# Kernel optimization log

Measured on AMD Instinct MI355X. Metric: run time of the kernel, lower is better.

Reference implementation:

```python
import jax, jax.numpy as jnp
import numpy as np

INPUT_DIM, HID_DIM, OUTPUT_DIM, N = 256, 128, 256, 16384
SCALE = 128 ** (-0.5)


def setup_inputs() -> dict:
    key = jax.random.key(0)
    ks = jax.random.split(key, 11)
    s_in = 1.0 / np.sqrt(INPUT_DIM)
    s_hid = 1.0 / np.sqrt(HID_DIM)
    return {
        "q": jax.random.normal(ks[0], (N, INPUT_DIM), jnp.float32),
        "k": jax.random.normal(ks[1], (N, INPUT_DIM), jnp.float32),
        "v": jax.random.normal(ks[2], (N, INPUT_DIM), jnp.float32),
        "Wq": jax.random.uniform(ks[3], (INPUT_DIM, HID_DIM), jnp.float32, -s_in, s_in),
        "bq": jax.random.uniform(ks[4], (HID_DIM,), jnp.float32, -s_in, s_in),
        "Wk": jax.random.uniform(ks[5], (INPUT_DIM, HID_DIM), jnp.float32, -s_in, s_in),
        "bk": jax.random.uniform(ks[6], (HID_DIM,), jnp.float32, -s_in, s_in),
        "Wv": jax.random.uniform(ks[7], (INPUT_DIM, HID_DIM), jnp.float32, -s_in, s_in),
        "bv": jax.random.uniform(ks[8], (HID_DIM,), jnp.float32, -s_in, s_in),
        "Wo": jax.random.uniform(ks[9], (HID_DIM, OUTPUT_DIM), jnp.float32, -s_hid, s_hid),
        "bo": jax.random.uniform(ks[10], (OUTPUT_DIM,), jnp.float32, -s_hid, s_hid),
    }


def reference(q, k, v, Wq, bq, Wk, bk, Wv, bv, Wo, bo):
    qh = q @ Wq + bq                      # [N, H]
    kh = k @ Wk + bk                      # [N, H]
    vh = v @ Wv + bv                      # [N, H]
    scores = (qh @ kh.T) * SCALE          # [N, N] materialized as in original
    attn = jax.nn.softmax(scores, axis=-1)
    out = attn @ vh                       # [N, H]
    return out @ Wo + bo                  # [N, OUTPUT_DIM]
```

## Files before the change

### kernel.cpp

```cpp
#include <hip/hip_runtime.h>
#include <hip/hip_bf16.h>
#include <stdint.h>


#define N_TOK 16384
#define IN_DIM 256
#define HID 128
#define OUT_DIM 256
#define KVB 32
#define BM 128
#define TOT_TILES (N_TOK / KVB)

typedef __bf16   bf16x8 __attribute__((ext_vector_type(8)));
typedef short    short8 __attribute__((ext_vector_type(8)));
typedef float    f32x4  __attribute__((ext_vector_type(4)));
typedef float    f32x16 __attribute__((ext_vector_type(16)));
typedef uint32_t u32x2  __attribute__((ext_vector_type(2)));
typedef long     longx2 __attribute__((ext_vector_type(2)));

#define MFMA16(a,b,c) __builtin_amdgcn_mfma_f32_16x16x32_bf16((a),(b),(c),0,0,0)
#define MFMA8(a,b,c)  __builtin_amdgcn_mfma_f32_32x32x16_fp8_fp8((a),(b),(c),0,0,0)
#define EXP2(x) __builtin_amdgcn_exp2f(x)

__device__ __forceinline__ short f2bf(float f) {
    union { float f; uint32_t u; } v; v.f = f;
    uint32_t r = v.u + 0x7FFFu + ((v.u >> 16) & 1u);
    return (short)(r >> 16);
}

template <bool HI>
__device__ __forceinline__ uint32_t pk_fp8(float a, float b, uint32_t old) {
    return (uint32_t)__builtin_amdgcn_cvt_pk_fp8_f32(a, b, (int)old, HI);
}

__device__ __forceinline__ unsigned char f2fp8(float f) {
    return (unsigned char)(pk_fp8<false>(f, f, 0u) & 0xFFu);
}

__device__ __forceinline__ void pswap(uint32_t& a, uint32_t& b) {
    auto r = __builtin_amdgcn_permlane32_swap(a, b, false, false);
    a = r[0]; b = r[1];
}

__device__ __forceinline__ void gl16(const void* g, const void* l) {
    __builtin_amdgcn_global_load_lds(
        (const __attribute__((address_space(1))) void*)g,
        (__attribute__((address_space(3))) void*)l, 16, 0, 0);
}

__global__ void wt4_kernel(const float* __restrict__ Wq, const float* __restrict__ Wk,
                           const float* __restrict__ Wv, const float* __restrict__ Wo,
                           short* __restrict__ tq, short* __restrict__ tk,
                           short* __restrict__ tv, short* __restrict__ to_)
{
    int idx = blockIdx.x * 256 + threadIdx.x;
    int w = idx >> 15, i = idx & 32767;
    if (w < 3) {
        const float* W = (w == 0) ? Wq : (w == 1) ? Wk : Wv;
        short* T = (w == 0) ? tq : (w == 1) ? tk : tv;
        int k = i >> 7, c = i & 127;
        T[c * 256 + k] = f2bf(W[i]);
    } else {
        int k = i >> 8, c = i & 255;
        to_[c * 128 + k] = f2bf(Wo[i]);
    }
}

__global__ __launch_bounds__(256) void proj3_kernel(
    const float* __restrict__ q, const float* __restrict__ k, const float* __restrict__ v,
    const short* __restrict__ tq, const short* __restrict__ tk, const short* __restrict__ tv,
    const float* __restrict__ bq, const float* __restrict__ bk, const float* __restrict__ bv,
    unsigned char* __restrict__ qh, unsigned char* __restrict__ kh,
    unsigned char* __restrict__ vh)
{
    const int y = blockIdx.y;
    const float* X  = (y == 0) ? q  : (y == 1) ? k  : v;
    const short* WT = (y == 0) ? tq : (y == 1) ? tk : tv;
    const float* bias = (y == 0) ? bq : (y == 1) ? bk : bv;
    unsigned char* Y = (y == 0) ? qh : (y == 1) ? kh : vh;

    const int lane = threadIdx.x & 63;
    const int wave = threadIdx.x >> 6;
    const int g = lane >> 4, c = lane & 15;
    const int rowbase = blockIdx.x * 64 + wave * 16;

    bf16x8 a[8];
    const float* xrow = X + (size_t)(rowbase + c) * IN_DIM;
#pragma unroll
    for (int kk = 0; kk < 8; ++kk) {
        const float* p = xrow + kk * 32 + 8 * g;
        float4 f0 = *(const float4*)(p);
        float4 f1 = *(const float4*)(p + 4);
        short8 t;
        t[0]=f2bf(f0.x); t[1]=f2bf(f0.y); t[2]=f2bf(f0.z); t[3]=f2bf(f0.w);
        t[4]=f2bf(f1.x); t[5]=f2bf(f1.y); t[6]=f2bf(f1.z); t[7]=f2bf(f1.w);
        a[kk] = __builtin_bit_cast(bf16x8, t);
    }

    f32x4 acc[8];
#pragma unroll
    for (int nf = 0; nf < 8; ++nf) acc[nf] = (f32x4){0.f, 0.f, 0.f, 0.f};

#pragma unroll
    for (int kk = 0; kk < 8; ++kk) {
#pragma unroll
        for (int nf = 0; nf < 8; ++nf) {
            bf16x8 b = *(const bf16x8*)(WT + (size_t)(c + 16 * nf) * IN_DIM + kk * 32 + 8 * g);
            acc[nf] = MFMA16(a[kk], b, acc[nf]);
        }
    }

#pragma unroll
    for (int nf = 0; nf < 8; ++nf) {
        int col = c + 16 * nf;
        float bval = bias[col];
#pragma unroll
        for (int r = 0; r < 4; ++r) {
            int row = rowbase + 4 * g + r;
            unsigned char val = f2fp8(acc[nf][r] + bval);
            if (y == 0) {
                Y[(size_t)row * HID + col] = val;
            } else if (y == 1) {
                Y[(size_t)(row >> 5) * 4096 + (col >> 5) * 1024 + ((col >> 3) & 1) * 512
                  + (row & 31) * 16 + ((col >> 4) & 1) * 8 + (col & 7)] = val;
            } else {
                Y[(size_t)(row >> 5) * 4096 + (col >> 5) * 1024 + ((row >> 3) & 1) * 512
                  + (col & 31) * 16 + ((row >> 4) & 1) * 8 + (row & 7)] = val;
            }
        }
    }
}

__global__ __launch_bounds__(256, 3) void flash_kernel(
    const unsigned char* __restrict__ qh, const unsigned char* __restrict__ kh,
    const unsigned char* __restrict__ vh,
    short* __restrict__ Opart, float* __restrict__ Lpart,
    int nsplit)
{
    __shared__ __align__(16) unsigned char K_lds[3][KVB * HID];
    __shared__ __align__(16) unsigned char V_lds[3][KVB * HID];

    const float kSc = 0.088388347648318447f * 1.4426950408889634f;

    const int tid  = threadIdx.x;
    const int lane = tid & 63;
    const int wave = tid >> 6;
    const int hi   = lane >> 5;
    const int col  = lane & 31;

    const int lid = blockIdx.x;
    const int split = lid >> 7;
    const int qtile = lid & 127;

    const int qb = qtile * BM + wave * 32;
    const int tbase = TOT_TILES / nsplit, trem = TOT_TILES % nsplit;
    const int ntiles = tbase + (split < trem ? 1 : 0);
    const int ktile0 = tbase * split + (split < trem ? split : trem);

    long qf[8];
    const unsigned char* qrow = qh + (size_t)(qb + col) * HID + 8 * hi;
#pragma unroll
    for (int kk = 0; kk < 8; ++kk)
        qf[kk] = *(const long*)(qrow + 16 * kk);

    f32x16 o[4];
#pragma unroll
    for (int nf = 0; nf < 4; ++nf)
#pragma unroll
        for (int i = 0; i < 16; ++i) o[nf][i] = 0.f;
    float l_run = 0.f;

    const unsigned char* kbase = kh + (size_t)ktile0 * 4096;
    const unsigned char* vbase = vh + (size_t)ktile0 * 4096;
    const int lds_off = tid * 16;
    const int frag_off = hi * 512 + col * 16;

    auto stage = [&](int t, int buf) {
        gl16(kbase + (size_t)t * 4096 + lds_off, &K_lds[buf][lds_off]);
        gl16(vbase + (size_t)t * 4096 + lds_off, &V_lds[buf][lds_off]);
    };

    stage(0, 0);
    if (1 < ntiles) stage(1, 1); else stage(0, 1);
    asm volatile("s_waitcnt vmcnt(2)" ::: "memory");
    __builtin_amdgcn_s_barrier();

    for (int t = 0; t < ntiles; ++t) {
        const int cur = t % 3;
        if (t + 2 < ntiles) stage(t + 2, (t + 2) % 3);
        const unsigned char* Kc = &K_lds[cur][0];
        const unsigned char* Vc = &V_lds[cur][0];

        f32x16 s0;
#pragma unroll
        for (int i = 0; i < 16; ++i) s0[i] = 0.f;
        __builtin_amdgcn_s_setprio(1);
#pragma unroll
        for (int p = 0; p < 4; ++p) {
            longx2 kp = *(const longx2*)(Kc + p * 1024 + frag_off);
            s0 = MFMA8(kp[0], qf[2 * p],     s0);
            s0 = MFMA8(kp[1], qf[2 * p + 1], s0);
        }
        __builtin_amdgcn_s_setprio(0);

        long pa0, pa1;
        {
            float e[16];
#pragma unroll
            for (int i = 0; i < 16; ++i) e[i] = EXP2(s0[i] * kSc);
            l_run += (((e[0]+e[1])+(e[2]+e[3])) + ((e[4]+e[5])+(e[6]+e[7])))
                   + (((e[8]+e[9])+(e[10]+e[11])) + ((e[12]+e[13])+(e[14]+e[15])));
            uint32_t A0 = pk_fp8<true>(e[2],  e[3],  pk_fp8<false>(e[0],  e[1],  0u));
            uint32_t B0 = pk_fp8<true>(e[6],  e[7],  pk_fp8<false>(e[4],  e[5],  0u));
            uint32_t A1 = pk_fp8<true>(e[10], e[11], pk_fp8<false>(e[8],  e[9],  0u));
            uint32_t B1 = pk_fp8<true>(e[14], e[15], pk_fp8<false>(e[12], e[13], 0u));
            pswap(A0, B0);
            pswap(A1, B1);
            pa0 = __builtin_bit_cast(long, (u32x2){A0, B0});
            pa1 = __builtin_bit_cast(long, (u32x2){A1, B1});
        }

        __builtin_amdgcn_s_setprio(1);
#pragma unroll
        for (int nf = 0; nf < 4; ++nf) {
            longx2 vp = *(const longx2*)(Vc + nf * 1024 + frag_off);
            o[nf] = MFMA8(pa0, vp[0], o[nf]);
            o[nf] = MFMA8(pa1, vp[1], o[nf]);
        }
        __builtin_amdgcn_s_setprio(0);

        if (t + 2 < ntiles)      asm volatile("s_waitcnt vmcnt(2)" ::: "memory");
        else if (t + 1 < ntiles) asm volatile("s_waitcnt vmcnt(0)" ::: "memory");
        __builtin_amdgcn_s_barrier();
    }

    {
        uint32_t ax = __builtin_bit_cast(uint32_t, l_run), bx = ax;
        pswap(ax, bx);
        l_run = __builtin_bit_cast(float, ax) + __builtin_bit_cast(float, bx);
    }
    const size_t sbase = (size_t)split * N_TOK + qb;
#pragma unroll
    for (int nf = 0; nf < 4; ++nf)
#pragma unroll
        for (int r = 0; r < 16; ++r) {
            int qr = (r & 3) + 8 * (r >> 2) + 4 * hi;
            Opart[(sbase + qr) * HID + 32 * nf + col] = f2bf(o[nf][r]);
        }
    if (lane < 32)
        Lpart[sbase + col] = l_run;
}

__global__ __launch_bounds__(256) void oproj_kernel(
    const short* __restrict__ Opart, const float* __restrict__ Lpart,
    const short* __restrict__ WoT, const float* __restrict__ bo,
    float* __restrict__ out, int nsplit)
{
    const int lane = threadIdx.x & 63;
    const int wave = threadIdx.x >> 6;
    const int g = lane >> 4, c = lane & 15;
    const int rowbase = blockIdx.x * 64 + wave * 16;
    const int row = rowbase + c;

    float denom = 0.f;
    for (int s = 0; s < nsplit; ++s) denom += Lpart[(size_t)s * N_TOK + row];
    const float inv = 1.0f / denom;

    float osum[4][8];
#pragma unroll
    for (int kk = 0; kk < 4; ++kk)
#pragma unroll
        for (int j = 0; j < 8; ++j) osum[kk][j] = 0.f;
    for (int s = 0; s < nsplit; ++s) {
        const short* orow = Opart + ((size_t)s * N_TOK + row) * HID;
#pragma unroll
        for (int kk = 0; kk < 4; ++kk) {
            bf16x8 vv = *(const bf16x8*)(orow + kk * 32 + 8 * g);
#pragma unroll
            for (int j = 0; j < 8; ++j) osum[kk][j] += (float)vv[j];
        }
    }
    bf16x8 a[4];
#pragma unroll
    for (int kk = 0; kk < 4; ++kk) {
        short8 t;
#pragma unroll
        for (int j = 0; j < 8; ++j) t[j] = f2bf(osum[kk][j] * inv);
        a[kk] = __builtin_bit_cast(bf16x8, t);
    }

    f32x4 acc[16];
#pragma unroll
    for (int nf = 0; nf < 16; ++nf) acc[nf] = (f32x4){0.f, 0.f, 0.f, 0.f};
#pragma unroll
    for (int kk = 0; kk < 4; ++kk)
#pragma unroll
        for (int nf = 0; nf < 16; ++nf) {
            bf16x8 b = *(const bf16x8*)(WoT + (size_t)(c + 16 * nf) * HID + kk * 32 + 8 * g);
            acc[nf] = MFMA16(a[kk], b, acc[nf]);
        }

#pragma unroll
    for (int nf = 0; nf < 16; ++nf) {
        int colo = c + 16 * nf;
        float bval = bo[colo];
#pragma unroll
        for (int r = 0; r < 4; ++r)
            out[(size_t)(rowbase + 4 * g + r) * OUT_DIM + colo] = acc[nf][r] + bval;
    }
}

extern "C" void kernel_launch(void* const* d_in, const int* in_sizes, int n_in,
                              void* d_out, int out_size, void* d_ws, size_t ws_size,
                              hipStream_t stream)
{
    (void)in_sizes; (void)n_in; (void)out_size;
    const float* q  = (const float*)d_in[0];
    const float* k  = (const float*)d_in[1];
    const float* v  = (const float*)d_in[2];
    const float* Wq = (const float*)d_in[3];
    const float* bq = (const float*)d_in[4];
    const float* Wk = (const float*)d_in[5];
    const float* bk = (const float*)d_in[6];
    const float* Wv = (const float*)d_in[7];
    const float* bvp= (const float*)d_in[8];
    const float* Wo = (const float*)d_in[9];
    const float* bo = (const float*)d_in[10];
    float* out = (float*)d_out;

    auto need = [](int ns) -> size_t {
        return (size_t)(4 * 65536)
             + (size_t)3 * N_TOK * HID
             + (size_t)ns * N_TOK * HID * 2
             + (size_t)ns * N_TOK * 4
             + (size_t)64 * 1024;
    };
    int nsplit = 6;
    if (ws_size < need(6)) nsplit = 4;
    if (ws_size < need(4)) nsplit = 2;
    if (ws_size < need(2)) nsplit = 1;

    char* base = (char*)d_ws;
    size_t off = 0;
    auto alloc = [&](size_t bytes) -> void* {
        void* p = base + off;
        off = (off + bytes + 255) & ~(size_t)255;
        return p;
    };
    short* wtq = (short*)alloc(128 * 256 * 2);
    short* wtk = (short*)alloc(128 * 256 * 2);
    short* wtv = (short*)alloc(128 * 256 * 2);
    short* wto = (short*)alloc(256 * 128 * 2);
    unsigned char* qh  = (unsigned char*)alloc((size_t)N_TOK * HID);
    unsigned char* khb = (unsigned char*)alloc((size_t)N_TOK * HID);
    unsigned char* vhb = (unsigned char*)alloc((size_t)N_TOK * HID);
    short* Opart = (short*)alloc((size_t)nsplit * N_TOK * HID * 2);
    float* Lp  = (float*)alloc((size_t)nsplit * N_TOK * 4);

    wt4_kernel<<<512, 256, 0, stream>>>(Wq, Wk, Wv, Wo, wtq, wtk, wtv, wto);

    proj3_kernel<<<dim3(N_TOK / 64, 3), 256, 0, stream>>>(
        q, k, v, wtq, wtk, wtv, bq, bk, bvp, qh, khb, vhb);

    flash_kernel<<<dim3(128 * nsplit), 256, 0, stream>>>(
        qh, khb, vhb, Opart, Lp, nsplit);

    oproj_kernel<<<N_TOK / 64, 256, 0, stream>>>(
        Opart, Lp, wto, bo, out, nsplit);
}
```

Baseline: 164.7 us.

## Use 64-key tiles with double buffering, higher occupancy and eight splits

The KV tile grows from 32 to 64 keys, processed as two 32-key halves per loop iteration. The LDS pipeline drops from triple to double buffering with a full vmcnt(0) wait each iteration, and launch bounds go from 3 to 4 blocks per CU. The split-K count rises from 6 to 8. The aim is to halve the barriers per key, raise occupancy and add parallelism, at the cost of a shallower prefetch and more partial outputs to reduce.

```diff
diff --git a/kernel.cpp b/kernel.cpp
--- a/kernel.cpp
+++ b/kernel.cpp
@@ -7,9 +7,9 @@
 #define IN_DIM 256
 #define HID 128
 #define OUT_DIM 256
-#define KVB 32
+#define KVB 64
 #define BM 128
-#define TOT_TILES (N_TOK / KVB)
+#define TT64 (N_TOK / KVB)
 
 typedef __bf16   bf16x8 __attribute__((ext_vector_type(8)));
 typedef short    short8 __attribute__((ext_vector_type(8)));
@@ -131,14 +131,14 @@
     }
 }
 
-__global__ __launch_bounds__(256, 3) void flash_kernel(
+__global__ __launch_bounds__(256, 4) void flash_kernel(
     const unsigned char* __restrict__ qh, const unsigned char* __restrict__ kh,
     const unsigned char* __restrict__ vh,
     short* __restrict__ Opart, float* __restrict__ Lpart,
     int nsplit)
 {
-    __shared__ __align__(16) unsigned char K_lds[3][KVB * HID];
-    __shared__ __align__(16) unsigned char V_lds[3][KVB * HID];
+    __shared__ __align__(16) unsigned char K_lds[2][KVB * HID];
+    __shared__ __align__(16) unsigned char V_lds[2][KVB * HID];
 
     const float kSc = 0.088388347648318447f * 1.4426950408889634f;
 
@@ -153,7 +153,7 @@
     const int qtile = lid & 127;
 
     const int qb = qtile * BM + wave * 32;
-    const int tbase = TOT_TILES / nsplit, trem = TOT_TILES % nsplit;
+    const int tbase = TT64 / nsplit, trem = TT64 % nsplit;
     const int ntiles = tbase + (split < trem ? 1 : 0);
     const int ktile0 = tbase * split + (split < trem ? split : trem);
 
@@ -170,67 +170,72 @@
         for (int i = 0; i < 16; ++i) o[nf][i] = 0.f;
     float l_run = 0.f;
 
-    const unsigned char* kbase = kh + (size_t)ktile0 * 4096;
-    const unsigned char* vbase = vh + (size_t)ktile0 * 4096;
+    const unsigned char* kbase = kh + (size_t)ktile0 * 8192;
+    const unsigned char* vbase = vh + (size_t)ktile0 * 8192;
     const int lds_off = tid * 16;
     const int frag_off = hi * 512 + col * 16;
 
     auto stage = [&](int t, int buf) {
-        gl16(kbase + (size_t)t * 4096 + lds_off, &K_lds[buf][lds_off]);
-        gl16(vbase + (size_t)t * 4096 + lds_off, &V_lds[buf][lds_off]);
+        const unsigned char* ks = kbase + (size_t)t * 8192 + lds_off;
+        const unsigned char* vs = vbase + (size_t)t * 8192 + lds_off;
+        gl16(ks,        &K_lds[buf][lds_off]);
+        gl16(ks + 4096, &K_lds[buf][4096 + lds_off]);
+        gl16(vs,        &V_lds[buf][lds_off]);
+        gl16(vs + 4096, &V_lds[buf][4096 + lds_off]);
     };
 
     stage(0, 0);
-    if (1 < ntiles) stage(1, 1); else stage(0, 1);
-    asm volatile("s_waitcnt vmcnt(2)" ::: "memory");
+    asm volatile("s_waitcnt vmcnt(0)" ::: "memory");
     __builtin_amdgcn_s_barrier();
 
     for (int t = 0; t < ntiles; ++t) {
-        const int cur = t % 3;
-        if (t + 2 < ntiles) stage(t + 2, (t + 2) % 3);
+        const int cur = t & 1;
+        if (t + 1 < ntiles) stage(t + 1, cur ^ 1);
         const unsigned char* Kc = &K_lds[cur][0];
         const unsigned char* Vc = &V_lds[cur][0];
 
-        f32x16 s0;
-#pragma unroll
-        for (int i = 0; i < 16; ++i) s0[i] = 0.f;
-        __builtin_amdgcn_s_setprio(1);
-#pragma unroll
-        for (int p = 0; p < 4; ++p) {
-            longx2 kp = *(const longx2*)(Kc + p * 1024 + frag_off);
-            s0 = MFMA8(kp[0], qf[2 * p],     s0);
-            s0 = MFMA8(kp[1], qf[2 * p + 1], s0);
-        }
-        __builtin_amdgcn_s_setprio(0);
-
-        long pa0, pa1;
-        {
-            float e[16];
-#pragma unroll
-            for (int i = 0; i < 16; ++i) e[i] = EXP2(s0[i] * kSc);
-            l_run += (((e[0]+e[1])+(e[2]+e[3])) + ((e[4]+e[5])+(e[6]+e[7])))
-                   + (((e[8]+e[9])+(e[10]+e[11])) + ((e[12]+e[13])+(e[14]+e[15])));
-            uint32_t A0 = pk_fp8<true>(e[2],  e[3],  pk_fp8<false>(e[0],  e[1],  0u));
-            uint32_t B0 = pk_fp8<true>(e[6],  e[7],  pk_fp8<false>(e[4],  e[5],  0u));
-            uint32_t A1 = pk_fp8<true>(e[10], e[11], pk_fp8<false>(e[8],  e[9],  0u));
-            uint32_t B1 = pk_fp8<true>(e[14], e[15], pk_fp8<false>(e[12], e[13], 0u));
-            pswap(A0, B0);
-            pswap(A1, B1);
-            pa0 = __builtin_bit_cast(long, (u32x2){A0, B0});
-            pa1 = __builtin_bit_cast(long, (u32x2){A1, B1});
-        }
-
-        __builtin_amdgcn_s_setprio(1);
-#pragma unroll
-        for (int nf = 0; nf < 4; ++nf) {
-            longx2 vp = *(const longx2*)(Vc + nf * 1024 + frag_off);
-            o[nf] = MFMA8(pa0, vp[0], o[nf]);
-            o[nf] = MFMA8(pa1, vp[1], o[nf]);
-        }
-        __builtin_amdgcn_s_setprio(0);
-
-        if (t + 2 < ntiles)      asm volatile("s_waitcnt vmcnt(2)" ::: "memory");
-        else if (t + 1 < ntiles) asm volatile("s_waitcnt vmcnt(0)" ::: "memory");
+#pragma unroll
+        for (int h = 0; h < 2; ++h) {
+            f32x16 s;
+#pragma unroll
+            for (int i = 0; i < 16; ++i) s[i] = 0.f;
+            __builtin_amdgcn_s_setprio(1);
+#pragma unroll
+            for (int p = 0; p < 4; ++p) {
+                longx2 kp = *(const longx2*)(Kc + h * 4096 + p * 1024 + frag_off);
+                s = MFMA8(kp[0], qf[2 * p],     s);
+                s = MFMA8(kp[1], qf[2 * p + 1], s);
+            }
+            __builtin_amdgcn_s_setprio(0);
+
+            long pa0, pa1;
+            {
+                float e[16];
+#pragma unroll
+                for (int i = 0; i < 16; ++i) e[i] = EXP2(s[i] * kSc);
+                l_run += (((e[0]+e[1])+(e[2]+e[3])) + ((e[4]+e[5])+(e[6]+e[7])))
+                       + (((e[8]+e[9])+(e[10]+e[11])) + ((e[12]+e[13])+(e[14]+e[15])));
+                uint32_t A0 = pk_fp8<true>(e[2],  e[3],  pk_fp8<false>(e[0],  e[1],  0u));
+                uint32_t B0 = pk_fp8<true>(e[6],  e[7],  pk_fp8<false>(e[4],  e[5],  0u));
+                uint32_t A1 = pk_fp8<true>(e[10], e[11], pk_fp8<false>(e[8],  e[9],  0u));
+                uint32_t B1 = pk_fp8<true>(e[14], e[15], pk_fp8<false>(e[12], e[13], 0u));
+                pswap(A0, B0);
+                pswap(A1, B1);
+                pa0 = __builtin_bit_cast(long, (u32x2){A0, B0});
+                pa1 = __builtin_bit_cast(long, (u32x2){A1, B1});
+            }
+
+            __builtin_amdgcn_s_setprio(1);
+#pragma unroll
+            for (int nf = 0; nf < 4; ++nf) {
+                longx2 vp = *(const longx2*)(Vc + h * 4096 + nf * 1024 + frag_off);
+                o[nf] = MFMA8(pa0, vp[0], o[nf]);
+                o[nf] = MFMA8(pa1, vp[1], o[nf]);
+            }
+            __builtin_amdgcn_s_setprio(0);
+        }
+
+        asm volatile("s_waitcnt vmcnt(0)" ::: "memory");
         __builtin_amdgcn_s_barrier();
     }
 
@@ -335,8 +340,8 @@
              + (size_t)ns * N_TOK * 4
              + (size_t)64 * 1024;
     };
-    int nsplit = 6;
-    if (ws_size < need(6)) nsplit = 4;
+    int nsplit = 8;
+    if (ws_size < need(8)) nsplit = 4;
     if (ws_size < need(4)) nsplit = 2;
     if (ws_size < need(2)) nsplit = 1;
 
```

After: 184.0 us. 1.12x slower.
